# Performance work log

Measured on AMD Instinct MI355X. Metric: run time of the kernel, lower is better.

The kernel has to match this reference:

```python
import jax, jax.numpy as jnp
import numpy as np

EMBED_DIM = 1024
NUM_HEADS = 16
HEAD_DIM = EMBED_DIM // NUM_HEADS


def setup_inputs() -> dict:
    key = jax.random.key(0)
    ks = jax.random.split(key, 12)
    B, S, D = 2, 2048, EMBED_DIM
    sc = 1.0 / np.sqrt(D)
    inp = {
        "query": jax.random.normal(ks[0], (B, S, D), jnp.float32),
        "key": jax.random.normal(ks[1], (B, S, D), jnp.float32),
        "value": jax.random.normal(ks[2], (B, S, D), jnp.float32),
        # causal mask: True = masked out (matches masked_fill semantics)
        "attn_mask": jnp.triu(jnp.ones((S, S), dtype=bool), k=1),
        "q_w": jax.random.normal(ks[3], (D, D), jnp.float32) * sc,
        "q_b": jnp.zeros((D,), jnp.float32),
        "k_w": jax.random.normal(ks[4], (D, D), jnp.float32) * sc,
        "k_b": jnp.zeros((D,), jnp.float32),
        "v_w": jax.random.normal(ks[5], (D, D), jnp.float32) * sc,
        "v_b": jnp.zeros((D,), jnp.float32),
        "o_w": jax.random.normal(ks[6], (D, D), jnp.float32) * sc,
        "o_b": jnp.zeros((D,), jnp.float32),
    }
    return inp


def reference(query, key, value, attn_mask, q_w, q_b, k_w, k_b, v_w, v_b, o_w, o_b):
    B, S, D = query.shape
    H, hd = NUM_HEADS, HEAD_DIM

    def proj(x, w, b):
        # nn.Linear: x @ w.T + b ; reshape to [B, H, S, hd]
        y = jnp.einsum('bsd,ed->bse', x, w) + b
        return y.reshape(B, S, H, hd).transpose(0, 2, 1, 3)

    Q = proj(query, q_w, q_b)
    K = proj(key, k_w, k_b)
    V = proj(value, v_w, v_b)

    scores = jnp.einsum('bhqd,bhkd->bhqk', Q, K) / jnp.sqrt(jnp.float32(hd))
    scores = jnp.where(attn_mask, jnp.float32(-1e9), scores)
    attn = jax.nn.softmax(scores, axis=-1)  # dropout=0.0 (eval)
    ctx = jnp.einsum('bhqk,bhkd->bhqd', attn, V)
    ctx = ctx.transpose(0, 2, 1, 3).reshape(B, S, D)
    out = jnp.einsum('bsd,ed->bse', ctx, o_w) + o_b
    return out
```

## Files before the change

### kernel.cpp

```cpp
#include <hip/hip_runtime.h>
#include <hip/hip_bf16.h>

typedef __bf16 bf16;
typedef __attribute__((ext_vector_type(8))) __bf16 bf16x8;
typedef __attribute__((ext_vector_type(4))) __bf16 bf16x4;
typedef __attribute__((ext_vector_type(4))) float f32x4;

struct CvtArgs {
  const float* src[7];
  bf16* dst[7];
  int n4[7];
};

__global__ __launch_bounds__(256) void cvt_kernel(CvtArgs a) {
  const int seg = blockIdx.y;
  const float4* s = (const float4*)a.src[seg];
  bf16x4* d = (bf16x4*)a.dst[seg];
  const int n = a.n4[seg];
  const int stride = gridDim.x * 256;
  for (int i = blockIdx.x * 256 + threadIdx.x; i < n; i += stride) {
    const float4 v = s[i];
    bf16x4 h;
    h[0] = (bf16)v.x; h[1] = (bf16)v.y; h[2] = (bf16)v.z; h[3] = (bf16)v.w;
    d[i] = h;
  }
}

__device__ __forceinline__ void gload16(const void* g, void* l) {
  __builtin_amdgcn_global_load_lds(
      (const __attribute__((address_space(1))) void*)g,
      (__attribute__((address_space(3))) void*)l, 16, 0, 0);
}

__device__ __forceinline__ void gemm_core(const bf16* __restrict__ A,
                                          const bf16* __restrict__ W,
                                          const float* __restrict__ bias,
                                          void* __restrict__ C,
                                          float scale, int mode) {
  constexpr int K = 1024, N = 1024;
  constexpr int BK = 64;
  __shared__ __align__(16) bf16 As[128 * BK];
  __shared__ __align__(16) bf16 Bs[128 * BK];

  const int tid = threadIdx.x;
  const int lane = tid & 63;
  const int w = tid >> 6;
  const int wr = w >> 1, wc = w & 1;
  const int g = lane >> 4, c16 = lane & 15;
  const int row0 = blockIdx.y * 128;
  const int col0 = blockIdx.x * 128;

  const int srow = tid >> 3;
  const int scol = (tid & 7) * 8;
  const int sdst = tid * 8;

  f32x4 acc[4][4] = {};

  for (int kt = 0; kt < K / BK; ++kt) {
    const int k0 = kt * BK;
    __syncthreads();
#pragma unroll
    for (int p = 0; p < 4; ++p) {
      gload16(&A[(size_t)(row0 + p * 32 + srow) * K + k0 + scol], &As[p * 2048 + sdst]);
      gload16(&W[(size_t)(col0 + p * 32 + srow) * K + k0 + scol], &Bs[p * 2048 + sdst]);
    }
    __syncthreads();

    bf16x8 a[4][2], b[4][2];
#pragma unroll
    for (int m = 0; m < 4; ++m)
#pragma unroll
      for (int ks = 0; ks < 2; ++ks)
        a[m][ks] = *(const bf16x8*)&As[(wr * 64 + m * 16 + c16) * BK + ks * 32 + g * 8];
#pragma unroll
    for (int n = 0; n < 4; ++n)
#pragma unroll
      for (int ks = 0; ks < 2; ++ks)
        b[n][ks] = *(const bf16x8*)&Bs[(wc * 64 + n * 16 + c16) * BK + ks * 32 + g * 8];
#pragma unroll
    for (int ks = 0; ks < 2; ++ks)
#pragma unroll
      for (int m = 0; m < 4; ++m)
#pragma unroll
        for (int n = 0; n < 4; ++n)
          acc[m][n] = __builtin_amdgcn_mfma_f32_16x16x32_bf16(a[m][ks], b[n][ks], acc[m][n], 0, 0, 0);
  }

#pragma unroll
  for (int m = 0; m < 4; ++m) {
#pragma unroll
    for (int n = 0; n < 4; ++n) {
      const int col = col0 + wc * 64 + n * 16 + c16;
      if (mode == 2) {
        const int row = row0 + wr * 64 + m * 16 + g * 4;
        const int bb = row >> 11, s = row & 2047;
        const int hh = col >> 6, j = col & 63;
        bf16x4 hv;
#pragma unroll
        for (int r = 0; r < 4; ++r)
          hv[r] = (bf16)((acc[m][n][r] + bias[col]) * scale);
        *(bf16x4*)&((bf16*)C)[(((size_t)bb * 16 + hh) * 64 + j) * 2048 + s] = hv;
      } else {
#pragma unroll
        for (int r = 0; r < 4; ++r) {
          const int row = row0 + wr * 64 + m * 16 + g * 4 + r;
          const float v = (acc[m][n][r] + bias[col]) * scale;
          if (mode == 1) {
            const int bb = row >> 11, s = row & 2047;
            const int hh = col >> 6, j = col & 63;
            ((bf16*)C)[(((size_t)bb * 16 + hh) * 2048 + s) * 64 + j] = (bf16)v;
          } else {
            ((float*)C)[(size_t)row * N + col] = v;
          }
        }
      }
    }
  }
}

__global__ __launch_bounds__(256) void qkv_gemm_kernel(
    const bf16* __restrict__ qa, const bf16* __restrict__ ka, const bf16* __restrict__ va,
    const bf16* __restrict__ qw, const bf16* __restrict__ kw, const bf16* __restrict__ vw,
    const float* __restrict__ qb, const float* __restrict__ kb, const float* __restrict__ vb,
    bf16* __restrict__ Qo, bf16* __restrict__ Ko, bf16* __restrict__ Vo, float qscale) {
  const int z = blockIdx.z;
  const bf16* A = (z == 0) ? qa : (z == 1) ? ka : va;
  const bf16* W = (z == 0) ? qw : (z == 1) ? kw : vw;
  const float* bias = (z == 0) ? qb : (z == 1) ? kb : vb;
  bf16* C = (z == 0) ? Qo : (z == 1) ? Ko : Vo;
  const float scale = (z == 0) ? qscale : 1.0f;
  const int mode = (z == 2) ? 2 : 1;
  gemm_core(A, W, bias, C, scale, mode);
}

__global__ __launch_bounds__(256) void o_gemm_kernel(
    const bf16* __restrict__ A, const bf16* __restrict__ W,
    const float* __restrict__ bias, float* __restrict__ C) {
  gemm_core(A, W, bias, C, 1.0f, 0);
}

template <bool A_BF16, int OUT_MODE>
__global__ __launch_bounds__(256) void gemm_bt_kernel(
    const void* __restrict__ Aptr, const float* __restrict__ Bt,
    const float* __restrict__ bias, void* __restrict__ Cptr, float scale) {
  constexpr int K = 1024, N = 1024;
  constexpr int BM = 128, BK = 32;
  constexpr int LSTR = BK + 8;
  __shared__ __align__(16) bf16 As[BM][LSTR];
  __shared__ __align__(16) bf16 Bs[BM][LSTR];

  const int tid = threadIdx.x;
  const int lane = tid & 63;
  const int w = tid >> 6;
  const int wr = w >> 1, wc = w & 1;
  const int g = lane >> 4, c16 = lane & 15;
  const int row0 = blockIdx.y * BM;
  const int col0 = blockIdx.x * BM;

  f32x4 acc[4][4] = {};

  for (int kt = 0; kt < K / BK; ++kt) {
    const int k0 = kt * BK;
    if constexpr (!A_BF16) {
      const float* A = (const float*)Aptr;
#pragma unroll
      for (int i = 0; i < 4; ++i) {
        const int r = (tid >> 3) + i * 32;
        const int c = (tid & 7) * 4;
        const float4 v = *(const float4*)(&A[(size_t)(row0 + r) * K + k0 + c]);
        bf16x4 hv;
        hv[0] = (bf16)v.x; hv[1] = (bf16)v.y; hv[2] = (bf16)v.z; hv[3] = (bf16)v.w;
        *(bf16x4*)&As[r][c] = hv;
      }
    } else {
      const bf16* A = (const bf16*)Aptr;
#pragma unroll
      for (int i = 0; i < 2; ++i) {
        const int r = (tid >> 2) + i * 64;
        const int c = (tid & 3) * 8;
        *(bf16x8*)&As[r][c] = *(const bf16x8*)(&A[(size_t)(row0 + r) * K + k0 + c]);
      }
    }
#pragma unroll
    for (int i = 0; i < 4; ++i) {
      const int r = (tid >> 3) + i * 32;
      const int c = (tid & 7) * 4;
      const float4 v = *(const float4*)(&Bt[(size_t)(col0 + r) * K + k0 + c]);
      bf16x4 hv;
      hv[0] = (bf16)v.x; hv[1] = (bf16)v.y; hv[2] = (bf16)v.z; hv[3] = (bf16)v.w;
      *(bf16x4*)&Bs[r][c] = hv;
    }
    __syncthreads();

    bf16x8 a[4], b[4];
#pragma unroll
    for (int m = 0; m < 4; ++m)
      a[m] = *(bf16x8*)&As[wr * 64 + m * 16 + c16][g * 8];
#pragma unroll
    for (int n = 0; n < 4; ++n)
      b[n] = *(bf16x8*)&Bs[wc * 64 + n * 16 + c16][g * 8];
#pragma unroll
    for (int m = 0; m < 4; ++m)
#pragma unroll
      for (int n = 0; n < 4; ++n)
        acc[m][n] = __builtin_amdgcn_mfma_f32_16x16x32_bf16(a[m], b[n], acc[m][n], 0, 0, 0);
    __syncthreads();
  }

#pragma unroll
  for (int m = 0; m < 4; ++m) {
#pragma unroll
    for (int n = 0; n < 4; ++n) {
      const int col = col0 + wc * 64 + n * 16 + c16;
      if constexpr (OUT_MODE == 2) {
        const int row = row0 + wr * 64 + m * 16 + g * 4;
        const int bb = row >> 11, s = row & 2047;
        const int hh = col >> 6, j = col & 63;
        bf16x4 hv;
#pragma unroll
        for (int r = 0; r < 4; ++r)
          hv[r] = (bf16)((acc[m][n][r] + bias[col]) * scale);
        *(bf16x4*)&((bf16*)Cptr)[(((size_t)bb * 16 + hh) * 64 + j) * 2048 + s] = hv;
      } else {
#pragma unroll
        for (int r = 0; r < 4; ++r) {
          const int row = row0 + wr * 64 + m * 16 + g * 4 + r;
          const float v = (acc[m][n][r] + bias[col]) * scale;
          if constexpr (OUT_MODE == 1) {
            const int bb = row >> 11, s = row & 2047;
            const int hh = col >> 6, j = col & 63;
            ((bf16*)Cptr)[(((size_t)bb * 16 + hh) * 2048 + s) * 64 + j] = (bf16)v;
          } else {
            ((float*)Cptr)[(size_t)row * N + col] = v;
          }
        }
      }
    }
  }
}

__global__ __launch_bounds__(256) void attn_kernel(
    const bf16* __restrict__ Q, const bf16* __restrict__ Kb,
    const bf16* __restrict__ Vt, bf16* __restrict__ ctx) {
  constexpr int S = 2048, HD = 64, KVB = 64;
  constexpr int PS = 72;
  __shared__ __align__(16) bf16 Ks[KVB][PS];
  __shared__ __align__(16) bf16 Vs[HD][PS];
  __shared__ __align__(16) bf16 PT[4][16][PS];

  const int tid = threadIdx.x;
  const int lane = tid & 63;
  const int w = tid >> 6;
  const int g = lane >> 4, c16 = lane & 15;
  const int bh = blockIdx.x;
  const int b = bh >> 4, h = bh & 15;

  const int jj = blockIdx.y;
  const int sub = jj & 7, grp = jj >> 3;
  const int qt = (grp == 0) ? sub : (grp == 1) ? 31 - sub : (grp == 2) ? 8 + sub : 23 - sub;

  const bf16* Qh = Q + (size_t)bh * S * HD;
  const bf16* Kh = Kb + (size_t)bh * S * HD;
  const bf16* Vh = Vt + (size_t)bh * HD * S;

  const int srow = tid >> 2;
  const int scol = (tid & 3) * 16;

  const int q0w = qt * 64 + w * 16;
  const int nt = qt + 1;

  bf16x8 qf[2];
#pragma unroll
  for (int ks = 0; ks < 2; ++ks)
    qf[ks] = *(const bf16x8*)&Qh[(size_t)(q0w + c16) * HD + ks * 32 + g * 8];

  f32x4 oacc[4] = {};
  float m = -1e30f, l = 0.f;

  bf16x8 kr0 = *(const bf16x8*)&Kh[(size_t)srow * HD + scol];
  bf16x8 kr1 = *(const bf16x8*)&Kh[(size_t)srow * HD + scol + 8];
  bf16x8 vr0 = *(const bf16x8*)&Vh[(size_t)srow * S + scol];
  bf16x8 vr1 = *(const bf16x8*)&Vh[(size_t)srow * S + scol + 8];

#pragma unroll 1
  for (int kt = 0; kt < nt; ++kt) {
    __syncthreads();
    *(bf16x8*)&Ks[srow][scol] = kr0;
    *(bf16x8*)&Ks[srow][scol + 8] = kr1;
    *(bf16x8*)&Vs[srow][scol] = vr0;
    *(bf16x8*)&Vs[srow][scol + 8] = vr1;
    __syncthreads();

    const int kv0 = kt * KVB;
    const bool pf = (kt + 1 < nt);
    if (pf) {
      const int nkv = kv0 + KVB;
      kr0 = *(const bf16x8*)&Kh[(size_t)(nkv + srow) * HD + scol];
      kr1 = *(const bf16x8*)&Kh[(size_t)(nkv + srow) * HD + scol + 8];
      vr0 = *(const bf16x8*)&Vh[(size_t)srow * S + nkv + scol];
      vr1 = *(const bf16x8*)&Vh[(size_t)srow * S + nkv + scol + 8];
    }

    f32x4 sc[4] = {};
    __builtin_amdgcn_s_setprio(1);
#pragma unroll
    for (int ks = 0; ks < 2; ++ks) {
#pragma unroll
      for (int ni = 0; ni < 4; ++ni) {
        const bf16x8 kf = *(const bf16x8*)&Ks[ni * 16 + c16][ks * 32 + g * 8];
        sc[ni] = __builtin_amdgcn_mfma_f32_16x16x32_bf16(kf, qf[ks], sc[ni], 0, 0, 0);
      }
    }
    __builtin_amdgcn_s_setprio(0);

    if (kt == qt) {
      const int qq = q0w + c16;
#pragma unroll
      for (int ni = 0; ni < 4; ++ni)
#pragma unroll
        for (int r = 0; r < 4; ++r) {
          const int kv = kv0 + ni * 16 + g * 4 + r;
          if (kv > qq) sc[ni][r] = -1e30f;
        }
    }

    float t = -1e30f;
#pragma unroll
    for (int ni = 0; ni < 4; ++ni)
#pragma unroll
      for (int r = 0; r < 4; ++r) t = fmaxf(t, sc[ni][r]);
    t = fmaxf(t, __shfl_xor(t, 16));
    t = fmaxf(t, __shfl_xor(t, 32));
    if (!__all(t <= m + 8.0f)) {
      const float mnew = fmaxf(m, t);
      const float corr = exp2f(m - mnew);
      m = mnew;
      l *= corr;
      float cb[4];
#pragma unroll
      for (int r = 0; r < 4; ++r)
        cb[r] = __shfl(corr, (lane & 48) + g * 4 + r);
#pragma unroll
      for (int nd = 0; nd < 4; ++nd)
#pragma unroll
        for (int r = 0; r < 4; ++r) oacc[nd][r] *= cb[r];
    }
    float rs = 0.f;
#pragma unroll
    for (int ni = 0; ni < 4; ++ni)
#pragma unroll
      for (int r = 0; r < 4; ++r) {
        sc[ni][r] = exp2f(sc[ni][r] - m);
        rs += sc[ni][r];
      }
    rs += __shfl_xor(rs, 16);
    rs += __shfl_xor(rs, 32);
    l += rs;

#pragma unroll
    for (int ni = 0; ni < 4; ++ni) {
      bf16x4 hv;
#pragma unroll
      for (int r = 0; r < 4; ++r) hv[r] = (bf16)sc[ni][r];
      *(bf16x4*)&PT[w][c16][ni * 16 + g * 4] = hv;
    }

    __builtin_amdgcn_s_setprio(1);
#pragma unroll
    for (int ks = 0; ks < 2; ++ks) {
      const bf16x8 pa = *(const bf16x8*)&PT[w][c16][ks * 32 + g * 8];
#pragma unroll
      for (int nd = 0; nd < 4; ++nd) {
        const bf16x8 bv = *(const bf16x8*)&Vs[nd * 16 + c16][ks * 32 + g * 8];
        oacc[nd] = __builtin_amdgcn_mfma_f32_16x16x32_bf16(pa, bv, oacc[nd], 0, 0, 0);
      }
    }
    __builtin_amdgcn_s_setprio(0);
  }

  float lb[4];
#pragma unroll
  for (int r = 0; r < 4; ++r)
    lb[r] = __shfl(l, (lane & 48) + g * 4 + r);
#pragma unroll
  for (int nd = 0; nd < 4; ++nd)
#pragma unroll
    for (int r = 0; r < 4; ++r) {
      const int q = q0w + g * 4 + r;
      const int col = h * 64 + nd * 16 + c16;
      ctx[((size_t)b * S + q) * 1024 + col] = (bf16)(oacc[nd][r] / lb[r]);
    }
}

extern "C" void kernel_launch(void* const* d_in, const int* in_sizes, int n_in,
                              void* d_out, int out_size, void* d_ws, size_t ws_size,
                              hipStream_t stream) {
  (void)in_sizes; (void)n_in; (void)out_size;
  const float* query = (const float*)d_in[0];
  const float* key   = (const float*)d_in[1];
  const float* value = (const float*)d_in[2];
  const float* q_w = (const float*)d_in[4];
  const float* q_b = (const float*)d_in[5];
  const float* k_w = (const float*)d_in[6];
  const float* k_b = (const float*)d_in[7];
  const float* v_w = (const float*)d_in[8];
  const float* v_b = (const float*)d_in[9];
  const float* o_w = (const float*)d_in[10];
  const float* o_b = (const float*)d_in[11];

  const size_t NELEM = (size_t)4096 * 1024;
  const size_t WELEM = (size_t)1024 * 1024;
  bf16* Qbuf = (bf16*)d_ws;
  bf16* Kbuf = Qbuf + NELEM;
  bf16* Vbuf = Kbuf + NELEM;
  bf16* ctxb = Vbuf + NELEM;

  const dim3 blk(256);
  const float QSCALE = 0.125f * 1.44269504088896f;

  const size_t need = 64ull * 1024 * 1024;
  if (ws_size >= need) {
    bf16* qbf  = ctxb + NELEM;
    bf16* kbf  = qbf + NELEM;
    bf16* vbf  = kbf + NELEM;
    bf16* qwbf = vbf + NELEM;
    bf16* kwbf = qwbf + WELEM;
    bf16* vwbf = kwbf + WELEM;
    bf16* owbf = vwbf + WELEM;

    CvtArgs ca;
    ca.src[0] = query; ca.dst[0] = qbf;  ca.n4[0] = (int)(NELEM / 4);
    ca.src[1] = key;   ca.dst[1] = kbf;  ca.n4[1] = (int)(NELEM / 4);
    ca.src[2] = value; ca.dst[2] = vbf;  ca.n4[2] = (int)(NELEM / 4);
    ca.src[3] = q_w;   ca.dst[3] = qwbf; ca.n4[3] = (int)(WELEM / 4);
    ca.src[4] = k_w;   ca.dst[4] = kwbf; ca.n4[4] = (int)(WELEM / 4);
    ca.src[5] = v_w;   ca.dst[5] = vwbf; ca.n4[5] = (int)(WELEM / 4);
    ca.src[6] = o_w;   ca.dst[6] = owbf; ca.n4[6] = (int)(WELEM / 4);
    cvt_kernel<<<dim3(256, 7), blk, 0, stream>>>(ca);

    qkv_gemm_kernel<<<dim3(8, 32, 3), blk, 0, stream>>>(
        qbf, kbf, vbf, qwbf, kwbf, vwbf, q_b, k_b, v_b, Qbuf, Kbuf, Vbuf, QSCALE);

    attn_kernel<<<dim3(32, 32), blk, 0, stream>>>(Qbuf, Kbuf, Vbuf, ctxb);

    o_gemm_kernel<<<dim3(8, 32), blk, 0, stream>>>(ctxb, owbf, o_b, (float*)d_out);
  } else {
    const dim3 ggrid(8, 32);
    gemm_bt_kernel<false, 1><<<ggrid, blk, 0, stream>>>(query, q_w, q_b, Qbuf, QSCALE);
    gemm_bt_kernel<false, 1><<<ggrid, blk, 0, stream>>>(key, k_w, k_b, Kbuf, 1.0f);
    gemm_bt_kernel<false, 2><<<ggrid, blk, 0, stream>>>(value, v_w, v_b, Vbuf, 1.0f);
    attn_kernel<<<dim3(32, 32), blk, 0, stream>>>(Qbuf, Kbuf, Vbuf, ctxb);
    gemm_bt_kernel<true, 0><<<ggrid, blk, 0, stream>>>(ctxb, o_w, o_b, d_out, 1.0f);
  }
}
```

Baseline: 144.9 us.

## Triple-buffer projection GEMM with swizzled LDS and XCD-aware block remapping

```diff
diff --git a/kernel.cpp b/kernel.cpp
--- a/kernel.cpp
+++ b/kernel.cpp
@@ -32,67 +32,85 @@
       (__attribute__((address_space(3))) void*)l, 16, 0, 0);
 }
 
-__device__ __forceinline__ void gemm_core(const bf16* __restrict__ A,
-                                          const bf16* __restrict__ W,
-                                          const float* __restrict__ bias,
-                                          void* __restrict__ C,
-                                          float scale, int mode) {
-  constexpr int K = 1024, N = 1024;
-  constexpr int BK = 64;
-  __shared__ __align__(16) bf16 As[128 * BK];
-  __shared__ __align__(16) bf16 Bs[128 * BK];
+__device__ __forceinline__ void gemm_core2(const bf16* __restrict__ A,
+                                           const bf16* __restrict__ W,
+                                           const float* __restrict__ bias,
+                                           void* __restrict__ C,
+                                           float scale, int mode,
+                                           int bx, int by) {
+  constexpr int K = 1024, N = 1024, BK = 32, NT = K / BK;
+  __shared__ __align__(16) bf16 As[3][128 * BK];
+  __shared__ __align__(16) bf16 Bs[3][128 * BK];
 
   const int tid = threadIdx.x;
   const int lane = tid & 63;
   const int w = tid >> 6;
-  const int wr = w >> 1, wc = w & 1;
+  const int wm = w >> 1, wn = w & 1;
   const int g = lane >> 4, c16 = lane & 15;
-  const int row0 = blockIdx.y * 128;
-  const int col0 = blockIdx.x * 128;
-
-  const int srow = tid >> 3;
-  const int scol = (tid & 7) * 8;
+  const int row0 = by * 128;
+  const int col0 = bx * 128;
+
+  const int sr = tid >> 2;
+  const int ssw = ((tid & 3) ^ (sr & 3)) * 8;
   const int sdst = tid * 8;
 
+  const int aoff = (wm * 64 + c16) * BK + ((g ^ (c16 & 3)) * 8);
+  const int boff = (wn * 64 + c16) * BK + ((g ^ (c16 & 3)) * 8);
+
   f32x4 acc[4][4] = {};
 
-  for (int kt = 0; kt < K / BK; ++kt) {
-    const int k0 = kt * BK;
-    __syncthreads();
-#pragma unroll
-    for (int p = 0; p < 4; ++p) {
-      gload16(&A[(size_t)(row0 + p * 32 + srow) * K + k0 + scol], &As[p * 2048 + sdst]);
-      gload16(&W[(size_t)(col0 + p * 32 + srow) * K + k0 + scol], &Bs[p * 2048 + sdst]);
-    }
-    __syncthreads();
-
-    bf16x8 a[4][2], b[4][2];
+#define STAGE2(buf, kt)                                                          \
+  {                                                                              \
+    const int k0_ = (kt)*BK;                                                     \
+    gload16(&A[(size_t)(row0 + sr) * K + k0_ + ssw], &As[buf][sdst]);            \
+    gload16(&A[(size_t)(row0 + 64 + sr) * K + k0_ + ssw], &As[buf][2048 + sdst]);\
+    gload16(&W[(size_t)(col0 + sr) * K + k0_ + ssw], &Bs[buf][sdst]);            \
+    gload16(&W[(size_t)(col0 + 64 + sr) * K + k0_ + ssw], &Bs[buf][2048 + sdst]);\
+  }
+
+  STAGE2(0, 0);
+  STAGE2(1, 1);
+
+  int cur = 0;
+#pragma unroll 1
+  for (int kt = 0; kt < NT; ++kt) {
+    if (kt == NT - 1)
+      asm volatile("s_waitcnt vmcnt(0)" ::: "memory");
+    else
+      asm volatile("s_waitcnt vmcnt(4)" ::: "memory");
+    __builtin_amdgcn_s_barrier();
+    __builtin_amdgcn_sched_barrier(0);
+
+    if (kt + 2 < NT) {
+      const int nb = (cur + 2 >= 3) ? cur - 1 : cur + 2;
+      STAGE2(nb, kt + 2);
+    }
+
+    bf16x8 a[4], b[4];
+#pragma unroll
+    for (int m = 0; m < 4; ++m) a[m] = *(const bf16x8*)&As[cur][aoff + m * 512];
+#pragma unroll
+    for (int n = 0; n < 4; ++n) b[n] = *(const bf16x8*)&Bs[cur][boff + n * 512];
+
+    __builtin_amdgcn_s_setprio(1);
 #pragma unroll
     for (int m = 0; m < 4; ++m)
 #pragma unroll
-      for (int ks = 0; ks < 2; ++ks)
-        a[m][ks] = *(const bf16x8*)&As[(wr * 64 + m * 16 + c16) * BK + ks * 32 + g * 8];
-#pragma unroll
-    for (int n = 0; n < 4; ++n)
-#pragma unroll
-      for (int ks = 0; ks < 2; ++ks)
-        b[n][ks] = *(const bf16x8*)&Bs[(wc * 64 + n * 16 + c16) * BK + ks * 32 + g * 8];
-#pragma unroll
-    for (int ks = 0; ks < 2; ++ks)
-#pragma unroll
-      for (int m = 0; m < 4; ++m)
-#pragma unroll
-        for (int n = 0; n < 4; ++n)
-          acc[m][n] = __builtin_amdgcn_mfma_f32_16x16x32_bf16(a[m][ks], b[n][ks], acc[m][n], 0, 0, 0);
-  }
+      for (int n = 0; n < 4; ++n)
+        acc[m][n] = __builtin_amdgcn_mfma_f32_16x16x32_bf16(a[m], b[n], acc[m][n], 0, 0, 0);
+    __builtin_amdgcn_s_setprio(0);
+
+    cur = (cur + 1 == 3) ? 0 : cur + 1;
+  }
+#undef STAGE2
 
 #pragma unroll
   for (int m = 0; m < 4; ++m) {
 #pragma unroll
     for (int n = 0; n < 4; ++n) {
-      const int col = col0 + wc * 64 + n * 16 + c16;
+      const int col = col0 + wn * 64 + n * 16 + c16;
       if (mode == 2) {
-        const int row = row0 + wr * 64 + m * 16 + g * 4;
+        const int row = row0 + wm * 64 + m * 16 + g * 4;
         const int bb = row >> 11, s = row & 2047;
         const int hh = col >> 6, j = col & 63;
         bf16x4 hv;
@@ -103,7 +121,7 @@
       } else {
 #pragma unroll
         for (int r = 0; r < 4; ++r) {
-          const int row = row0 + wr * 64 + m * 16 + g * 4 + r;
+          const int row = row0 + wm * 64 + m * 16 + g * 4 + r;
           const float v = (acc[m][n][r] + bias[col]) * scale;
           if (mode == 1) {
             const int bb = row >> 11, s = row & 2047;
@@ -118,25 +136,37 @@
   }
 }
 
-__global__ __launch_bounds__(256) void qkv_gemm_kernel(
+__device__ __forceinline__ void xcd_swz(int& bx, int& by, int& bz) {
+  const int lid = ((int)blockIdx.z * 32 + (int)blockIdx.y) * 8 + (int)blockIdx.x;
+  const int cpx = ((int)gridDim.z * 256) >> 3;
+  int s = (lid & 7) * cpx + (lid >> 3);
+  bx = s & 7;
+  by = (s >> 3) & 31;
+  bz = s >> 8;
+}
+
+__global__ __launch_bounds__(256, 3) void qkv_gemm_kernel(
     const bf16* __restrict__ qa, const bf16* __restrict__ ka, const bf16* __restrict__ va,
     const bf16* __restrict__ qw, const bf16* __restrict__ kw, const bf16* __restrict__ vw,
     const float* __restrict__ qb, const float* __restrict__ kb, const float* __restrict__ vb,
     bf16* __restrict__ Qo, bf16* __restrict__ Ko, bf16* __restrict__ Vo, float qscale) {
-  const int z = blockIdx.z;
-  const bf16* A = (z == 0) ? qa : (z == 1) ? ka : va;
-  const bf16* W = (z == 0) ? qw : (z == 1) ? kw : vw;
-  const float* bias = (z == 0) ? qb : (z == 1) ? kb : vb;
-  bf16* C = (z == 0) ? Qo : (z == 1) ? Ko : Vo;
-  const float scale = (z == 0) ? qscale : 1.0f;
-  const int mode = (z == 2) ? 2 : 1;
-  gemm_core(A, W, bias, C, scale, mode);
-}
-
-__global__ __launch_bounds__(256) void o_gemm_kernel(
+  int bx, by, bz;
+  xcd_swz(bx, by, bz);
+  const bf16* A = (bz == 0) ? qa : (bz == 1) ? ka : va;
+  const bf16* W = (bz == 0) ? qw : (bz == 1) ? kw : vw;
+  const float* bias = (bz == 0) ? qb : (bz == 1) ? kb : vb;
+  bf16* C = (bz == 0) ? Qo : (bz == 1) ? Ko : Vo;
+  const float scale = (bz == 0) ? qscale : 1.0f;
+  const int mode = (bz == 2) ? 2 : 1;
+  gemm_core2(A, W, bias, C, scale, mode, bx, by);
+}
+
+__global__ __launch_bounds__(256, 3) void o_gemm_kernel(
     const bf16* __restrict__ A, const bf16* __restrict__ W,
     const float* __restrict__ bias, float* __restrict__ C) {
-  gemm_core(A, W, bias, C, 1.0f, 0);
+  int bx, by, bz;
+  xcd_swz(bx, by, bz);
+  gemm_core2(A, W, bias, C, 1.0f, 0, bx, by);
 }
 
 template <bool A_BF16, int OUT_MODE>
```

Measured after the change: 124.6 us. 14.0% less time.
